# Kernel tuning notes

Hardware: AMD Instinct MI355X
Metric: run time of the kernel (lower is better)

## Reference

```python
import jax, jax.numpy as jnp
import numpy as np

NUM_HEADS = 16


def _make_rope(n, half_dim, dtype=jnp.float32):
    # standard rotary frequencies: theta = 10000^{-2i/d}
    inv_freq = 1.0 / (10000.0 ** (np.arange(0, half_dim, dtype=np.float32) / half_dim))
    t = np.arange(n, dtype=np.float32)
    ang = np.outer(t, inv_freq)  # [n, half_dim]
    return jnp.asarray(np.cos(ang), dtype), jnp.asarray(np.sin(ang), dtype)


def setup_inputs() -> dict:
    key = jax.random.key(0)
    ks = jax.random.split(key, 10)
    B, N, C = 2, 2048, 1024
    H = NUM_HEADS
    hd = C // H
    q = jax.random.normal(ks[0], (B, N, C), jnp.float32)
    k = jax.random.normal(ks[1], (B, N, C), jnp.float32)
    v = jax.random.normal(ks[2], (B, N, C), jnp.float32)
    cos, sin = _make_rope(N, hd // 2)
    s = 1.0 / np.sqrt(C)
    Wq = jax.random.normal(ks[3], (C, C), jnp.float32) * s
    bq = jax.random.normal(ks[4], (C,), jnp.float32) * 0.02
    Wk = jax.random.normal(ks[5], (C, C), jnp.float32) * s
    bk = jax.random.normal(ks[6], (C,), jnp.float32) * 0.02
    Wv = jax.random.normal(ks[7], (C, C), jnp.float32) * s
    bv = jax.random.normal(ks[8], (C,), jnp.float32) * 0.02
    return {"q": q, "k": k, "v": v,
            "q_cos": cos, "q_sin": sin, "k_cos": cos, "k_sin": sin,
            "Wq": Wq, "bq": bq, "Wk": Wk, "bk": bk, "Wv": Wv, "bv": bv}


def _rope(x, cos, sin):
    # x: [B, H, N, hd]; pairs (x[...,2j], x[...,2j+1]) form complex numbers,
    # rotated by freqs_cis of shape [N, hd//2] (broadcast over B, H).
    xr = x[..., 0::2]
    xi = x[..., 1::2]
    c = cos[None, None]  # [1,1,N,hd//2]
    s = sin[None, None]
    out_r = xr * c - xi * s
    out_i = xr * s + xi * c
    return jnp.stack([out_r, out_i], axis=-1).reshape(x.shape)


def reference(q, k, v, q_cos, q_sin, k_cos, k_sin, Wq, bq, Wk, bk, Wv, bv):
    B, Nq, C = q.shape
    Nk = k.shape[1]
    H = NUM_HEADS
    hd = C // H
    scale = hd ** -0.5
    # QKV projections (torch nn.Linear: x @ W.T + b), split into heads
    qh = (q @ Wq.T + bq).reshape(B, Nq, H, hd).transpose(0, 2, 1, 3)  # [B,H,Nq,hd]
    kh = (k @ Wk.T + bk).reshape(B, Nk, H, hd).transpose(0, 2, 1, 3)
    vh = (v @ Wv.T + bv).reshape(B, Nk, H, hd).transpose(0, 2, 1, 3)
    # inline RoPE on q and k
    qh = _rope(qh, q_cos, q_sin)
    kh = _rope(kh, k_cos, k_sin)
    # scaled dot-product attention (mask=None, dropout=0, non-causal)
    scores = jnp.einsum('bhqd,bhkd->bhqk', qh, kh) * scale
    attn = jax.nn.softmax(scores, axis=-1)
    out = jnp.einsum('bhqk,bhkd->bhqd', attn, vh)
    # merge heads; NOTE: self.proj is never applied in the original forward
    return out.transpose(0, 2, 1, 3).reshape(B, Nq, C)
```

## Files before the change

### kernel.cpp

```cpp
#include <hip/hip_runtime.h>
#include <hip/hip_bf16.h>

typedef float f32x4 __attribute__((ext_vector_type(4)));
typedef float f32x16 __attribute__((ext_vector_type(16)));
typedef short bf16x8 __attribute__((ext_vector_type(8)));

#define NSEQ 2048
#define CDIM 1024
#define NHEAD 16
#define HDIM 64
#define MROWS 4096
#define QSCALE 0.18033688011f
#define DEFER_THR 11.5416f

__device__ __forceinline__ unsigned short f2bf(float f) {
    unsigned int u = __builtin_bit_cast(unsigned int, f);
    u += 0x7FFFu + ((u >> 16) & 1u);
    return (unsigned short)(u >> 16);
}

__device__ __forceinline__ unsigned pkbf(float lo, float hi_) {
    unsigned r;
    asm("v_cvt_pk_bf16_f32 %0, %1, %2" : "=v"(r) : "v"(lo), "v"(hi_));
    return r;
}

__device__ __forceinline__ void gload16(const void* g, void* l) {
    __builtin_amdgcn_global_load_lds(
        (const __attribute__((address_space(1))) unsigned int*)g,
        (__attribute__((address_space(3))) unsigned int*)l, 16, 0, 0);
}

__global__ __launch_bounds__(256) void cvt6_kernel(
    const float* __restrict__ q, const float* __restrict__ k, const float* __restrict__ v,
    const float* __restrict__ wq, const float* __restrict__ wk, const float* __restrict__ wv,
    unsigned short* __restrict__ dq, unsigned short* __restrict__ dk, unsigned short* __restrict__ dv,
    unsigned short* __restrict__ dwq, unsigned short* __restrict__ dwk, unsigned short* __restrict__ dwv)
{
    int b = blockIdx.x;
    const float* s; unsigned short* d; int base;
    if (b < 4096)       { s = q;  d = dq;  base = b; }
    else if (b < 8192)  { s = k;  d = dk;  base = b - 4096; }
    else if (b < 12288) { s = v;  d = dv;  base = b - 8192; }
    else if (b < 13312) { s = wq; d = dwq; base = b - 12288; }
    else if (b < 14336) { s = wk; d = dwk; base = b - 13312; }
    else                { s = wv; d = dwv; base = b - 14336; }
    int i = (base * 256 + threadIdx.x) * 4;
    float4 t4 = *reinterpret_cast<const float4*>(s + i);
    ushort4 o;
    o.x = f2bf(t4.x); o.y = f2bf(t4.y); o.z = f2bf(t4.z); o.w = f2bf(t4.w);
    *reinterpret_cast<ushort4*>(d + i) = o;
}

__global__ __launch_bounds__(256) void gemm_rope_kernel(
    const unsigned short* __restrict__ Xq, const unsigned short* __restrict__ Xk,
    const unsigned short* __restrict__ Xv,
    const unsigned short* __restrict__ Wqb, const unsigned short* __restrict__ Wkb,
    const unsigned short* __restrict__ Wvb,
    const float* __restrict__ bq, const float* __restrict__ bk, const float* __restrict__ bv,
    const float* __restrict__ qcos, const float* __restrict__ qsin,
    const float* __restrict__ kcos, const float* __restrict__ ksin,
    unsigned short* __restrict__ Qh, unsigned short* __restrict__ Kh,
    unsigned short* __restrict__ VT)
{
    __shared__ unsigned short Al[128][72];
    __shared__ unsigned short Bl[128][72];

    const int tid  = threadIdx.x;
    const int wave = tid >> 6;
    const int lane = tid & 63;
    const int lr   = lane & 15;
    const int lg   = lane >> 4;
    const int lk   = lg * 8;
    const int wm   = wave >> 1;
    const int wn   = wave & 1;
    const int m0   = blockIdx.y * 128;
    const int j0   = blockIdx.x * 128;
    const int z    = blockIdx.z;

    const unsigned short* X = (z == 0) ? Xq : (z == 1) ? Xk : Xv;
    const unsigned short* W = (z == 0) ? Wqb : (z == 1) ? Wkb : Wvb;
    const float* bias = (z == 0) ? bq : (z == 1) ? bk : bv;
    const float* cosb = (z == 0) ? qcos : kcos;
    const float* sinb = (z == 0) ? qsin : ksin;

    f32x4 acc[4][4];
    const f32x4 zero4 = {0.f, 0.f, 0.f, 0.f};
    #pragma unroll
    for (int a = 0; a < 4; a++)
        #pragma unroll
        for (int b = 0; b < 4; b++) acc[a][b] = zero4;

    for (int k0 = 0; k0 < CDIM; k0 += 64) {
        __syncthreads();
        #pragma unroll
        for (int it = 0; it < 4; it++) {
            int c = tid + it * 256;
            int row = c >> 3, col = (c & 7) << 3;
            *reinterpret_cast<bf16x8*>(&Al[row][col]) =
                *reinterpret_cast<const bf16x8*>(X + (size_t)(m0 + row) * CDIM + k0 + col);
            *reinterpret_cast<bf16x8*>(&Bl[row][col]) =
                *reinterpret_cast<const bf16x8*>(W + (size_t)(j0 + row) * CDIM + k0 + col);
        }
        __syncthreads();
        #pragma unroll
        for (int ks = 0; ks < 2; ks++) {
            bf16x8 af[4], bfm[4];
            #pragma unroll
            for (int mi = 0; mi < 4; mi++)
                af[mi] = *reinterpret_cast<const bf16x8*>(&Al[wm * 64 + 16 * mi + lr][ks * 32 + lk]);
            #pragma unroll
            for (int ni = 0; ni < 4; ni++)
                bfm[ni] = *reinterpret_cast<const bf16x8*>(&Bl[wn * 64 + 16 * ni + lr][ks * 32 + lk]);
            #pragma unroll
            for (int mi = 0; mi < 4; mi++)
                #pragma unroll
                for (int ni = 0; ni < 4; ni++)
                    acc[mi][ni] = __builtin_amdgcn_mfma_f32_16x16x32_bf16(
                        af[mi], bfm[ni], acc[mi][ni], 0, 0, 0);
        }
    }

    #pragma unroll
    for (int mi = 0; mi < 4; mi++) {
        const int mbase = m0 + wm * 64 + 16 * mi + 4 * lg;
        #pragma unroll
        for (int ni = 0; ni < 4; ni++) {
            const int j  = j0 + wn * 64 + 16 * ni + lr;
            const float bj = bias[j];
            if (z == 2) {
                const int b = mbase >> 11, n = mbase & 2047;
                const int h = j >> 6, d = j & 63;
                ushort4 pk;
                pk.x = f2bf(acc[mi][ni][0] + bj);
                pk.y = f2bf(acc[mi][ni][1] + bj);
                pk.z = f2bf(acc[mi][ni][2] + bj);
                pk.w = f2bf(acc[mi][ni][3] + bj);
                *reinterpret_cast<ushort4*>(VT + ((size_t)((b * NHEAD + h) * HDIM + d) << 11) + n) = pk;
            } else {
                unsigned short* Out = (z == 0) ? Qh : Kh;
                const float scl = (z == 0) ? QSCALE : 1.0f;
                const int hi = (j & 63) >> 1;
                const float sg = (j & 1) ? 1.f : -1.f;
                float vv[4], pp[4];
                #pragma unroll
                for (int r = 0; r < 4; r++) vv[r] = acc[mi][ni][r] + bj;
                #pragma unroll
                for (int r = 0; r < 4; r++) pp[r] = __shfl_xor(vv[r], 1);
                #pragma unroll
                for (int r = 0; r < 4; r++) {
                    const int m = mbase + r;
                    const int b = m >> 11, n = m & 2047;
                    const float c = cosb[n * 32 + hi];
                    const float s = sinb[n * 32 + hi];
                    const float ov = fmaf(vv[r], c, pp[r] * (sg * s)) * scl;
                    Out[((size_t)((b * NHEAD + (j >> 6)) * NSEQ + n) << 6) + (j & 63)] = f2bf(ov);
                }
            }
        }
    }
}

__global__ __launch_bounds__(256, 4) void attn_kernel(
    const unsigned short* __restrict__ Qh, const unsigned short* __restrict__ Kh,
    const unsigned short* __restrict__ VT, float* __restrict__ out,
    float* __restrict__ O2, float2* __restrict__ ML)
{
    __shared__ unsigned char Ksm[2][4096];
    __shared__ unsigned char Vsm[2][4096];

    const int tid  = threadIdx.x;
    const int wave = tid >> 6;
    const int lane = tid & 63;
    const int c    = lane & 31;
    const int hi   = lane >> 5;
    const int bh   = blockIdx.x;
    const int q0w  = blockIdx.y * 128 + wave * 32;
    const int half = blockIdx.z;
    const int kbase = half * 1024;
    const int sw   = (c & 7) << 4;

    const unsigned short* Qb = Qh + (size_t)bh * NSEQ * HDIM;
    const char* Kb = (const char*)(Kh + (size_t)bh * NSEQ * HDIM);
    const char* Vb = (const char*)(VT + (size_t)bh * HDIM * NSEQ);

    bf16x8 qf[4];
    #pragma unroll
    for (int s = 0; s < 4; s++)
        qf[s] = *reinterpret_cast<const bf16x8*>(
            Qb + (size_t)(q0w + c) * HDIM + s * 16 + hi * 8);

    const f32x16 z16 = {0,0,0,0,0,0,0,0,0,0,0,0,0,0,0,0};
    f32x16 o0 = z16, o1 = z16;
    float mrun = -1e30f, lrun = 0.f;

    const int srow = wave * 8 + (lane >> 3);
    const int lb   = ((lane & 7) * 16) ^ ((srow & 7) << 4);
    const size_t skoff = (size_t)srow * 128 + lb;
    const int dv   = (lb & 64) ? (srow + 32) : srow;
    const size_t svoff = (size_t)dv * (NSEQ * 2) + (lb & 63);

    auto stage = [&](int buf, int n0) {
        gload16(Kb + (size_t)n0 * 128 + skoff, &Ksm[buf][wave * 1024]);
        gload16(Vb + (size_t)n0 * 2 + svoff, &Vsm[buf][wave * 1024]);
    };

    stage(0, kbase);
    __syncthreads();
    int cur = 0;

    for (int t = 0; t < 32; ++t) {
        if (t < 31) stage(cur ^ 1, kbase + (t + 1) * 32);

        f32x16 s = z16;
        __builtin_amdgcn_s_setprio(1);
        #pragma unroll
        for (int si = 0; si < 4; si++) {
            bf16x8 kf = *reinterpret_cast<const bf16x8*>(
                &Ksm[cur][c * 128 + ((si * 32 + hi * 16) ^ sw)]);
            s = __builtin_amdgcn_mfma_f32_32x32x16_bf16(kf, qf[si], s, 0, 0, 0);
        }
        __builtin_amdgcn_s_setprio(0);

        float tmx[8];
        #pragma unroll
        for (int i = 0; i < 8; i++) tmx[i] = fmaxf(s[2 * i], s[2 * i + 1]);
        float tm = fmaxf(fmaxf(fmaxf(tmx[0], tmx[1]), fmaxf(tmx[2], tmx[3])),
                         fmaxf(fmaxf(tmx[4], tmx[5]), fmaxf(tmx[6], tmx[7])));
        tm = fmaxf(tm, __shfl_xor(tm, 32));

        if (!__all(tm - mrun <= DEFER_THR)) {
            const float mnew  = fmaxf(mrun, tm);
            const float alpha = exp2f(mrun - mnew);
            mrun = mnew;
            lrun *= alpha;
            #pragma unroll
            for (int r = 0; r < 16; r++) {
                const float ar = __shfl(alpha, (r & 3) + 8 * (r >> 2) + 4 * hi);
                o0[r] *= ar;
                o1[r] *= ar;
            }
        }

        #pragma unroll
        for (int r = 0; r < 16; r++) s[r] = exp2f(s[r] - mrun);
        float rsx[8];
        #pragma unroll
        for (int i = 0; i < 8; i++) rsx[i] = s[2 * i] + s[2 * i + 1];
        float rs = ((rsx[0] + rsx[1]) + (rsx[2] + rsx[3])) +
                   ((rsx[4] + rsx[5]) + (rsx[6] + rsx[7]));
        rs += __shfl_xor(rs, 32);
        lrun += rs;

        unsigned pw[2][4];
        #pragma unroll
        for (int u = 0; u < 2; u++) {
            const int b = u * 8;
            unsigned x0 = pkbf(s[b + 0], s[b + 1]);
            unsigned y0 = pkbf(s[b + 4], s[b + 5]);
            asm("v_permlane32_swap_b32 %0, %1" : "+v"(x0), "+v"(y0));
            unsigned x1 = pkbf(s[b + 2], s[b + 3]);
            unsigned y1 = pkbf(s[b + 6], s[b + 7]);
            asm("v_permlane32_swap_b32 %0, %1" : "+v"(x1), "+v"(y1));
            pw[u][0] = x0; pw[u][1] = x1; pw[u][2] = y0; pw[u][3] = y1;
        }

        __builtin_amdgcn_s_setprio(1);
        #pragma unroll
        for (int u = 0; u < 2; u++) {
            uint4 w;
            w.x = pw[u][0]; w.y = pw[u][1]; w.z = pw[u][2]; w.w = pw[u][3];
            bf16x8 pa = __builtin_bit_cast(bf16x8, w);
            bf16x8 vf0 = *reinterpret_cast<const bf16x8*>(
                &Vsm[cur][c * 128 + ((u * 32 + hi * 16) ^ sw)]);
            bf16x8 vf1 = *reinterpret_cast<const bf16x8*>(
                &Vsm[cur][c * 128 + ((64 + u * 32 + hi * 16) ^ sw)]);
            o0 = __builtin_amdgcn_mfma_f32_32x32x16_bf16(pa, vf0, o0, 0, 0, 0);
            o1 = __builtin_amdgcn_mfma_f32_32x32x16_bf16(pa, vf1, o1, 0, 0, 0);
        }
        __builtin_amdgcn_s_setprio(0);

        __syncthreads();
        cur ^= 1;
    }

    float* obase = half ? O2 : out;
    const int b = bh >> 4, h = bh & 15;
    #pragma unroll
    for (int r = 0; r < 16; r++) {
        const int qrow = (r & 3) + 8 * (r >> 2) + 4 * hi;
        const int n = q0w + qrow;
        float* op = obase + ((size_t)(b * NSEQ + n) << 10) + h * HDIM + c;
        op[0]  = o0[r];
        op[32] = o1[r];
    }
    if (hi == 0)
        ML[((size_t)half * 32 + bh) * NSEQ + q0w + c] = make_float2(mrun, lrun);
}

__global__ __launch_bounds__(256) void attn_combine(
    float* __restrict__ out, const float* __restrict__ O2,
    const float2* __restrict__ ML)
{
    const int idx4 = blockIdx.x * 256 + threadIdx.x;
    const int e    = idx4 * 4;
    const int row  = e >> 10;
    const int col  = e & 1023;
    const int h    = col >> 6;
    const int b    = row >> 11;
    const int n    = row & 2047;
    const int bh   = b * NHEAD + h;

    const float2 ml1 = ML[(size_t)bh * NSEQ + n];
    const float2 ml2 = ML[((size_t)32 + bh) * NSEQ + n];
    const float M  = fmaxf(ml1.x, ml2.x);
    const float w1 = exp2f(ml1.x - M);
    const float w2 = exp2f(ml2.x - M);
    const float inv = 1.0f / (w1 * ml1.y + w2 * ml2.y);

    float4 a = reinterpret_cast<float4*>(out)[idx4];
    float4 d = reinterpret_cast<const float4*>(O2)[idx4];
    float4 r;
    r.x = (w1 * a.x + w2 * d.x) * inv;
    r.y = (w1 * a.y + w2 * d.y) * inv;
    r.z = (w1 * a.z + w2 * d.z) * inv;
    r.w = (w1 * a.w + w2 * d.w) * inv;
    reinterpret_cast<float4*>(out)[idx4] = r;
}

extern "C" void kernel_launch(void* const* d_in, const int* in_sizes, int n_in,
                              void* d_out, int out_size, void* d_ws, size_t ws_size,
                              hipStream_t stream) {
    const float* q    = (const float*)d_in[0];
    const float* k    = (const float*)d_in[1];
    const float* v    = (const float*)d_in[2];
    const float* qcos = (const float*)d_in[3];
    const float* qsin = (const float*)d_in[4];
    const float* kcos = (const float*)d_in[5];
    const float* ksin = (const float*)d_in[6];
    const float* Wq   = (const float*)d_in[7];
    const float* bq   = (const float*)d_in[8];
    const float* Wk   = (const float*)d_in[9];
    const float* bk   = (const float*)d_in[10];
    const float* Wv   = (const float*)d_in[11];
    const float* bv   = (const float*)d_in[12];
    float* out = (float*)d_out;

    unsigned short* Xqb = (unsigned short*)d_ws;
    unsigned short* Xkb = Xqb + (size_t)MROWS * CDIM;
    unsigned short* Xvb = Xkb + (size_t)MROWS * CDIM;
    unsigned short* Wqb = Xvb + (size_t)MROWS * CDIM;
    unsigned short* Wkb = Wqb + (size_t)CDIM * CDIM;
    unsigned short* Wvb = Wkb + (size_t)CDIM * CDIM;
    unsigned short* Qhb = Wvb + (size_t)CDIM * CDIM;
    unsigned short* Khb = Qhb + (size_t)MROWS * CDIM;
    unsigned short* VTb = Khb + (size_t)MROWS * CDIM;

    float*  O2 = (float*)Xqb;
    float2* ML = (float2*)((char*)d_ws + (size_t)16 * 1024 * 1024);

    cvt6_kernel<<<15360, 256, 0, stream>>>(q, k, v, Wq, Wk, Wv,
                                           Xqb, Xkb, Xvb, Wqb, Wkb, Wvb);

    dim3 gg(CDIM / 128, MROWS / 128, 3);
    gemm_rope_kernel<<<gg, 256, 0, stream>>>(Xqb, Xkb, Xvb, Wqb, Wkb, Wvb,
                                             bq, bk, bv, qcos, qsin, kcos, ksin,
                                             Qhb, Khb, VTb);

    attn_kernel<<<dim3(2 * NHEAD, NSEQ / 128, 2), 256, 0, stream>>>(
        Qhb, Khb, VTb, out, O2, ML);

    attn_combine<<<(MROWS * CDIM / 4) / 256, 256, 0, stream>>>(out, O2, ML);
}
```

Measured before the change: 140.4 us.

## Load K/V fragments directly from global memory instead of LDS staging

Removes the double-buffered LDS staging of K and V tiles, the async global-to-LDS loads and the per-iteration block barrier in the attention kernel. Each wave now loads its K and V MFMA operands straight from global memory, with the loop unrolled by two to give some latency hiding. This drops the LDS traffic and synchronisation, but each of the four waves in a block now fetches the same K/V data separately, relying on cache hits. Load latency is also exposed without explicit prefetch.

```diff
diff --git a/kernel.cpp b/kernel.cpp
--- a/kernel.cpp
+++ b/kernel.cpp
@@ -23,12 +23,6 @@
     unsigned r;
     asm("v_cvt_pk_bf16_f32 %0, %1, %2" : "=v"(r) : "v"(lo), "v"(hi_));
     return r;
-}
-
-__device__ __forceinline__ void gload16(const void* g, void* l) {
-    __builtin_amdgcn_global_load_lds(
-        (const __attribute__((address_space(1))) unsigned int*)g,
-        (__attribute__((address_space(3))) unsigned int*)l, 16, 0, 0);
 }
 
 __global__ __launch_bounds__(256) void cvt6_kernel(
@@ -166,9 +160,6 @@
     const unsigned short* __restrict__ VT, float* __restrict__ out,
     float* __restrict__ O2, float2* __restrict__ ML)
 {
-    __shared__ unsigned char Ksm[2][4096];
-    __shared__ unsigned char Vsm[2][4096];
-
     const int tid  = threadIdx.x;
     const int wave = tid >> 6;
     const int lane = tid & 63;
@@ -178,7 +169,6 @@
     const int q0w  = blockIdx.y * 128 + wave * 32;
     const int half = blockIdx.z;
     const int kbase = half * 1024;
-    const int sw   = (c & 7) << 4;
 
     const unsigned short* Qb = Qh + (size_t)bh * NSEQ * HDIM;
     const char* Kb = (const char*)(Kh + (size_t)bh * NSEQ * HDIM);
@@ -194,32 +184,31 @@
     f32x16 o0 = z16, o1 = z16;
     float mrun = -1e30f, lrun = 0.f;
 
-    const int srow = wave * 8 + (lane >> 3);
-    const int lb   = ((lane & 7) * 16) ^ ((srow & 7) << 4);
-    const size_t skoff = (size_t)srow * 128 + lb;
-    const int dv   = (lb & 64) ? (srow + 32) : srow;
-    const size_t svoff = (size_t)dv * (NSEQ * 2) + (lb & 63);
-
-    auto stage = [&](int buf, int n0) {
-        gload16(Kb + (size_t)n0 * 128 + skoff, &Ksm[buf][wave * 1024]);
-        gload16(Vb + (size_t)n0 * 2 + svoff, &Vsm[buf][wave * 1024]);
-    };
-
-    stage(0, kbase);
-    __syncthreads();
-    int cur = 0;
-
+    const char* kp  = Kb + (size_t)(kbase + c) * 128 + hi * 16;
+    const char* vp0 = Vb + (size_t)c * (NSEQ * 2) + (size_t)kbase * 2 + hi * 16;
+    const char* vp1 = vp0 + (size_t)32 * (NSEQ * 2);
+
+    #pragma unroll 2
     for (int t = 0; t < 32; ++t) {
-        if (t < 31) stage(cur ^ 1, kbase + (t + 1) * 32);
+        const char* kt  = kp  + (size_t)t * (32 * 128);
+        const char* vt0 = vp0 + t * 64;
+        const char* vt1 = vp1 + t * 64;
+
+        bf16x8 kf0 = *reinterpret_cast<const bf16x8*>(kt);
+        bf16x8 kf1 = *reinterpret_cast<const bf16x8*>(kt + 32);
+        bf16x8 kf2 = *reinterpret_cast<const bf16x8*>(kt + 64);
+        bf16x8 kf3 = *reinterpret_cast<const bf16x8*>(kt + 96);
+        bf16x8 va0 = *reinterpret_cast<const bf16x8*>(vt0);
+        bf16x8 va1 = *reinterpret_cast<const bf16x8*>(vt0 + 32);
+        bf16x8 vb0 = *reinterpret_cast<const bf16x8*>(vt1);
+        bf16x8 vb1 = *reinterpret_cast<const bf16x8*>(vt1 + 32);
 
         f32x16 s = z16;
         __builtin_amdgcn_s_setprio(1);
-        #pragma unroll
-        for (int si = 0; si < 4; si++) {
-            bf16x8 kf = *reinterpret_cast<const bf16x8*>(
-                &Ksm[cur][c * 128 + ((si * 32 + hi * 16) ^ sw)]);
-            s = __builtin_amdgcn_mfma_f32_32x32x16_bf16(kf, qf[si], s, 0, 0, 0);
-        }
+        s = __builtin_amdgcn_mfma_f32_32x32x16_bf16(kf0, qf[0], s, 0, 0, 0);
+        s = __builtin_amdgcn_mfma_f32_32x32x16_bf16(kf1, qf[1], s, 0, 0, 0);
+        s = __builtin_amdgcn_mfma_f32_32x32x16_bf16(kf2, qf[2], s, 0, 0, 0);
+        s = __builtin_amdgcn_mfma_f32_32x32x16_bf16(kf3, qf[3], s, 0, 0, 0);
         __builtin_amdgcn_s_setprio(0);
 
         float tmx[8];
@@ -266,22 +255,17 @@
         }
 
         __builtin_amdgcn_s_setprio(1);
-        #pragma unroll
-        for (int u = 0; u < 2; u++) {
-            uint4 w;
-            w.x = pw[u][0]; w.y = pw[u][1]; w.z = pw[u][2]; w.w = pw[u][3];
-            bf16x8 pa = __builtin_bit_cast(bf16x8, w);
-            bf16x8 vf0 = *reinterpret_cast<const bf16x8*>(
-                &Vsm[cur][c * 128 + ((u * 32 + hi * 16) ^ sw)]);
-            bf16x8 vf1 = *reinterpret_cast<const bf16x8*>(
-                &Vsm[cur][c * 128 + ((64 + u * 32 + hi * 16) ^ sw)]);
-            o0 = __builtin_amdgcn_mfma_f32_32x32x16_bf16(pa, vf0, o0, 0, 0, 0);
-            o1 = __builtin_amdgcn_mfma_f32_32x32x16_bf16(pa, vf1, o1, 0, 0, 0);
+        {
+            uint4 w0; w0.x = pw[0][0]; w0.y = pw[0][1]; w0.z = pw[0][2]; w0.w = pw[0][3];
+            bf16x8 pa0 = __builtin_bit_cast(bf16x8, w0);
+            o0 = __builtin_amdgcn_mfma_f32_32x32x16_bf16(pa0, va0, o0, 0, 0, 0);
+            o1 = __builtin_amdgcn_mfma_f32_32x32x16_bf16(pa0, vb0, o1, 0, 0, 0);
+            uint4 w1; w1.x = pw[1][0]; w1.y = pw[1][1]; w1.z = pw[1][2]; w1.w = pw[1][3];
+            bf16x8 pa1 = __builtin_bit_cast(bf16x8, w1);
+            o0 = __builtin_amdgcn_mfma_f32_32x32x16_bf16(pa1, va1, o0, 0, 0, 0);
+            o1 = __builtin_amdgcn_mfma_f32_32x32x16_bf16(pa1, vb1, o1, 0, 0, 0);
         }
         __builtin_amdgcn_s_setprio(0);
-
-        __syncthreads();
-        cur ^= 1;
     }
 
     float* obase = half ? O2 : out;
```

New measurement: 198.9 us. 41.7% more time.
